# Performance work log

Measured on AMD Instinct MI355X. Metric: run time of the kernel, lower is better.

## Reference

```python
import jax, jax.numpy as jnp
import numpy as np

B, N, H, A, S = 8, 8192, 256, 64, 32  # batch, nodes, hidden, annotation, sub_graphs


def _mysoftmax(x):
    # exp, zero out where x <= 0, normalize over last dim, nan (0/0) -> 0
    x_exp = jnp.where(x > 0, jnp.exp(x), 0.0)
    part = jnp.sum(x_exp, axis=-1, keepdims=True)
    # safe divide: where partition == 0 the faithful result after nan_to_num is 0
    return jnp.where(part > 0, x_exp / jnp.where(part > 0, part, 1.0), 0.0)


def setup_inputs() -> dict:
    key = jax.random.key(0)
    k1, k2, k3, k4, k5, k6 = jax.random.split(key, 6)
    x = jax.random.normal(k1, (B, N, H + A), dtype=jnp.float32)
    node_map = jax.random.uniform(k2, (B, S, N), dtype=jnp.float32)
    lim = 1.0 / np.sqrt(H + A)
    Wi = jax.random.uniform(k3, (H, H + A), minval=-lim, maxval=lim, dtype=jnp.float32)
    bi = jax.random.uniform(k4, (H,), minval=-lim, maxval=lim, dtype=jnp.float32)
    Wj = jax.random.uniform(k5, (H, H + A), minval=-lim, maxval=lim, dtype=jnp.float32)
    bj = jax.random.uniform(k6, (H,), minval=-lim, maxval=lim, dtype=jnp.float32)
    return {"x": x, "node_map": node_map, "Wi": Wi, "bi": bi, "Wj": Wj, "bj": bj}


def reference(x, node_map, Wi, bi, Wj, bj):
    # gated node features: sigmoid(fc_i(x)) * tanh(fc_j(x))  -> [B, N, H]
    x_sigm = jax.nn.sigmoid(jnp.einsum('bnf,hf->bnh', x, Wi) + bi)
    x_tanh = jnp.tanh(jnp.einsum('bnf,hf->bnh', x, Wj) + bj)
    x_all = x_sigm * x_tanh
    # per-node L2 norm -> [B, 1, N]
    x_norm = jnp.linalg.norm(x_all, axis=-1)[:, None, :]
    # scaled subgraph map and masked softmax over nodes -> [B, S, N]
    weight = _mysoftmax(node_map * x_norm)
    # weighted sum over nodes (replaces [B,S,N,H] broadcast) -> [B, S, H]
    pooled = jnp.einsum('bsn,bnh->bsh', weight, x_all)
    return jnp.tanh(pooled), weight[..., None]
```

## Files before the change

### kernel.cpp

```cpp
#include <hip/hip_runtime.h>
#include <cstdint>
#include <cstddef>

typedef unsigned short u16;
typedef unsigned int   u32;
using short8 = __attribute__((ext_vector_type(8))) short;
using f32x4  = __attribute__((ext_vector_type(4))) float;

#define NB    8
#define NN    8192
#define HH    256
#define FF    320
#define SS    32
#define NROWS 65536
#define NCH   32

__device__ __forceinline__ u16 f2bf(float f) {
    union { float f; u32 u; } v; v.f = f;
    u32 r = v.u + 0x7fffu + ((v.u >> 16) & 1u);
    return (u16)(r >> 16);
}
__device__ __forceinline__ u32 pk2(float lo, float hi) {
    u32 r;
    asm("v_cvt_pk_bf16_f32 %0, %1, %2" : "=v"(r) : "v"(lo), "v"(hi));
    return r;
}

__global__ __launch_bounds__(256) void prep_all(
    const float* __restrict__ x, const float* __restrict__ Wi,
    const float* __restrict__ Wj,
    u16* __restrict__ xb16, u16* __restrict__ Wb, float* __restrict__ normsq)
{
    int gid = blockIdx.x * 256 + threadIdx.x;
    #pragma unroll
    for (int i = 0; i < 5; ++i) {
        size_t o = (size_t)gid + (size_t)i * 524288;
        const float4* s = reinterpret_cast<const float4*>(x + o * 8);
        float4 a = s[0], b = s[1];
        union { u32 u[4]; uint4 v; } r;
        r.u[0] = pk2(a.x, a.y); r.u[1] = pk2(a.z, a.w);
        r.u[2] = pk2(b.x, b.y); r.u[3] = pk2(b.z, b.w);
        *reinterpret_cast<uint4*>(xb16 + o * 8) = r.v;
    }
    if (gid < 163840) {
        float v = (gid < 81920) ? Wi[gid] : Wj[gid - 81920];
        Wb[gid] = f2bf(v);
    }
    if (gid < NROWS) normsq[gid] = 0.f;
}

__global__ __launch_bounds__(256, 2) void gemm_gate(
    const u16* __restrict__ xb16, const u16* __restrict__ Wb,
    const float* __restrict__ bi, const float* __restrict__ bj,
    u16* __restrict__ xa, float* __restrict__ normsq)
{
    __shared__ u16 lB[5 * 8192];

    const int bx   = blockIdx.x;
    const int xcd  = bx & 7;
    const int ht   = (bx >> 3) & 3;
    const int slot = bx >> 5;
    const int mb   = xcd + slot * 8;
    const int m0   = mb * 256;
    const int h0   = ht * 64;
    const int b_idx = m0 >> 13;
    const int n0    = m0 & 8191;

    const int tid  = threadIdx.x;
    const int w    = tid >> 6;
    const int lane = tid & 63;
    const int quad = lane >> 4;
    const int l15  = lane & 15;

    {
        const int rsub = lane >> 3;
        const int kg   = (lane & 7) ^ rsub;
        #pragma unroll
        for (int kt = 0; kt < 5; ++kt) {
            #pragma unroll
            for (int j = 0; j < 4; ++j) {
                int sl  = w * 4 + j;
                int row = sl * 8 + rsub;
                int mat = row >> 6, hl = row & 63;
                const u16* gsrc = Wb + mat * 81920 + (size_t)(h0 + hl) * FF + kt * 64 + kg * 8;
                u16* ldst = &lB[kt * 8192 + sl * 512];
                __builtin_amdgcn_global_load_lds(
                    (const __attribute__((address_space(1))) void*)gsrc,
                    (__attribute__((address_space(3))) void*)ldst, 16, 0, 0);
            }
        }
    }

    const u16* xb = xb16 + (size_t)(m0 + w * 64 + l15) * FF + quad * 8;

    f32x4 acc[8][4];
    #pragma unroll
    for (int a = 0; a < 8; ++a)
        #pragma unroll
        for (int m = 0; m < 4; ++m) acc[a][m] = (f32x4){0.f, 0.f, 0.f, 0.f};

    short8 pre[4][4];
    #pragma unroll
    for (int p = 0; p < 3; ++p)
        #pragma unroll
        for (int mt = 0; mt < 4; ++mt)
            pre[p][mt] = *reinterpret_cast<const short8*>(xb + mt * 16 * FF + p * 32);

    __syncthreads();

    #pragma unroll
    for (int ks = 0; ks < 10; ++ks) {
        const int cur = ks & 3;
        if (ks < 7) {
            const int nxt = (ks + 3) & 3;
            const int f   = (ks + 3) * 32;
            #pragma unroll
            for (int mt = 0; mt < 4; ++mt)
                pre[nxt][mt] = *reinterpret_cast<const short8*>(xb + mt * 16 * FF + f);
        }
        const int kt = ks >> 1, kk = ks & 1;
        #pragma unroll
        for (int mn = 0; mn < 8; ++mn) {
            int c = mn * 16 + l15;
            short8 bv = *reinterpret_cast<const short8*>(
                &lB[kt * 8192 + c * 64 + (((kk * 4 + quad) ^ (c & 7)) << 3)]);
            #pragma unroll
            for (int mt = 0; mt < 4; ++mt)
                acc[mn][mt] = __builtin_amdgcn_mfma_f32_16x16x32_bf16(pre[cur][mt], bv, acc[mn][mt], 0, 0, 0);
        }
    }

    float s0[4][4];
    #pragma unroll
    for (int mt = 0; mt < 4; ++mt)
        #pragma unroll
        for (int r = 0; r < 4; ++r) s0[mt][r] = 0.f;

    #pragma unroll
    for (int hq = 0; hq < 4; ++hq) {
        int h = h0 + hq * 16 + l15;
        float bi_v = bi[h], bj_v = bj[h];
        #pragma unroll
        for (int mt = 0; mt < 4; ++mt) {
            float xall[4];
            #pragma unroll
            for (int r = 0; r < 4; ++r) {
                float yi = acc[hq][mt][r] + bi_v;
                float yj = acc[hq + 4][mt][r] + bj_v;
                float sg = 1.f / (1.f + __expf(-yi));
                float e2 = __expf(-2.f * yj);
                float th = (1.f - e2) / (1.f + e2);
                float xv = sg * th;
                xall[r] = xv;
                s0[mt][r] += xv * xv;
            }
            uint2 pk;
            pk.x = pk2(xall[0], xall[1]);
            pk.y = pk2(xall[2], xall[3]);
            size_t o = (size_t)b_idx * ((size_t)HH * NN) + (size_t)h * NN
                     + (size_t)(n0 + w * 64 + mt * 16 + quad * 4);
            *reinterpret_cast<uint2*>(&xa[o]) = pk;
        }
    }
    #pragma unroll
    for (int m = 1; m <= 8; m <<= 1) {
        #pragma unroll
        for (int mt = 0; mt < 4; ++mt)
            #pragma unroll
            for (int r = 0; r < 4; ++r)
                s0[mt][r] += __shfl_xor(s0[mt][r], m, 64);
    }
    if (l15 == 0) {
        #pragma unroll
        for (int mt = 0; mt < 4; ++mt)
            #pragma unroll
            for (int r = 0; r < 4; ++r)
                atomicAdd(&normsq[m0 + w * 64 + mt * 16 + quad * 4 + r], s0[mt][r]);
    }
}

__global__ __launch_bounds__(1024) void softmax_k(
    const float* __restrict__ nm, const float* __restrict__ normsq,
    float* __restrict__ out1)
{
    __shared__ float red[16];
    int bs = blockIdx.x;
    int b  = bs >> 5;
    const float* src = nm + (size_t)bs * NN;
    float* dst       = out1 + (size_t)bs * NN;
    const float* ns  = normsq + (size_t)b * NN;
    int tid = threadIdx.x;
    float e[8];
    float sum = 0.f;
    #pragma unroll
    for (int i = 0; i < 8; ++i) {
        int n = i * 1024 + tid;
        float logit = src[n] * sqrtf(ns[n]);
        float v = (logit > 0.f) ? __expf(logit) : 0.f;
        e[i] = v;
        sum += v;
    }
    #pragma unroll
    for (int m = 1; m <= 32; m <<= 1) sum += __shfl_xor(sum, m, 64);
    int w = tid >> 6, lane = tid & 63;
    if (lane == 0) red[w] = sum;
    __syncthreads();
    float part = 0.f;
    #pragma unroll
    for (int j = 0; j < 16; ++j) part += red[j];
    float inv = (part > 0.f) ? (1.f / part) : 0.f;
    #pragma unroll
    for (int i = 0; i < 8; ++i) dst[i * 1024 + tid] = e[i] * inv;
}

__global__ __launch_bounds__(256) void pooled_k(
    const u16* __restrict__ xa, const float* __restrict__ wgt,
    float* __restrict__ part)
{
    __shared__ u16 lw[32 * 264];
    int bx = blockIdx.x;
    int ht = bx >> 8;
    int bc = bx & 255;
    int b  = bc >> 5, c = bc & 31;
    int n0 = c * 256;
    int tid = threadIdx.x, w = tid >> 6, lane = tid & 63, quad = lane >> 4, l15 = lane & 15;

    {
        int s  = tid >> 3;
        int nb = (tid & 7) * 32;
        const float* src = wgt + (size_t)(b * SS + s) * NN + n0 + nb;
        #pragma unroll
        for (int q = 0; q < 8; ++q) {
            float4 v = *reinterpret_cast<const float4*>(src + q * 4);
            uint2 pk;
            pk.x = pk2(v.x, v.y);
            pk.y = pk2(v.z, v.w);
            *reinterpret_cast<uint2*>(&lw[s * 264 + nb + q * 4]) = pk;
        }
    }
    __syncthreads();

    f32x4 acc[2];
    acc[0] = (f32x4){0.f, 0.f, 0.f, 0.f};
    acc[1] = (f32x4){0.f, 0.f, 0.f, 0.f};

    const u16* ab = xa + (size_t)b * ((size_t)HH * NN)
                  + (size_t)(ht * 64 + w * 16 + l15) * NN + n0;
    #pragma unroll
    for (int ks = 0; ks < 8; ++ks) {
        short8 av = *reinterpret_cast<const short8*>(ab + ks * 32 + quad * 8);
        #pragma unroll
        for (int st = 0; st < 2; ++st) {
            int s = st * 16 + l15;
            short8 bv = *reinterpret_cast<const short8*>(&lw[s * 264 + ks * 32 + quad * 8]);
            acc[st] = __builtin_amdgcn_mfma_f32_16x16x32_bf16(av, bv, acc[st], 0, 0, 0);
        }
    }
    float* pb = part + (size_t)(b * NCH + c) * 8192;
    #pragma unroll
    for (int st = 0; st < 2; ++st) {
        int h = ht * 64 + w * 16 + quad * 4;
        int s = st * 16 + l15;
        *reinterpret_cast<f32x4*>(&pb[s * 256 + h]) = acc[st];
    }
}

__global__ __launch_bounds__(256) void reduce_tanh(const float* __restrict__ part,
                                                   float* __restrict__ out0)
{
    int gid = blockIdx.x * 256 + threadIdx.x;
    int b = gid >> 13, r = gid & 8191;
    const float* p = part + (size_t)b * NCH * 8192 + r;
    float s = 0.f;
    #pragma unroll
    for (int c = 0; c < NCH; ++c) s += p[(size_t)c * 8192];
    out0[gid] = tanhf(s);
}

extern "C" void kernel_launch(void* const* d_in, const int* in_sizes, int n_in,
                              void* d_out, int out_size, void* d_ws, size_t ws_size,
                              hipStream_t stream) {
    const float* x  = (const float*)d_in[0];
    const float* nm = (const float*)d_in[1];
    const float* Wi = (const float*)d_in[2];
    const float* bi = (const float*)d_in[3];
    const float* Wj = (const float*)d_in[4];
    const float* bj = (const float*)d_in[5];
    float* out0 = (float*)d_out;
    float* out1 = out0 + NB * SS * HH;

    char* ws = (char*)d_ws;
    u16*   Wb     = (u16*)ws;
    u16*   xb16   = (u16*)(ws + 327680);
    u16*   xa     = (u16*)(ws + 327680 + 41943040);
    float* normsq = (float*)(ws + 327680 + 41943040 + 33554432);
    float* part   = (float*)(ws + 327680 + 41943040 + 33554432 + 262144);

    prep_all   <<<2048, 256, 0, stream>>>(x, Wi, Wj, xb16, Wb, normsq);
    gemm_gate  <<<1024, 256, 0, stream>>>(xb16, Wb, bi, bj, xa, normsq);
    softmax_k  <<<256, 1024, 0, stream>>>(nm, normsq, out1);
    pooled_k   <<<1024, 256, 0, stream>>>(xa, out1, part);
    reduce_tanh<<<256,  256, 0, stream>>>(part, out0);
}
```

Before: 199.5 us.

## Emit bf16 softmax weights once and read them directly in pooled kernel

The softmax kernel now also writes a bf16 copy of the weights, and switches to contiguous 8-element float4 loads and stores per thread. The pooled kernel reads those bf16 weights straight from global memory as MFMA operands, with no LDS staging, no per-block fp32-to-bf16 conversion and no __syncthreads. Before, the weights were read four times as fp32 (once per h-tile block). The cost is an extra workspace buffer, an extra write in softmax, and uncached-pattern global loads for the B operand in pooled_k.

New measurement: 204.8 us. +2.7%, slower.

```diff
diff --git a/kernel.cpp b/kernel.cpp
--- a/kernel.cpp
+++ b/kernel.cpp
@@ -181,21 +181,28 @@
 
 __global__ __launch_bounds__(1024) void softmax_k(
     const float* __restrict__ nm, const float* __restrict__ normsq,
-    float* __restrict__ out1)
+    float* __restrict__ out1, u16* __restrict__ wgtb)
 {
     __shared__ float red[16];
     int bs = blockIdx.x;
     int b  = bs >> 5;
     const float* src = nm + (size_t)bs * NN;
     float* dst       = out1 + (size_t)bs * NN;
+    u16* dstb        = wgtb + (size_t)bs * NN;
     const float* ns  = normsq + (size_t)b * NN;
     int tid = threadIdx.x;
+    int n0  = tid * 8;
     float e[8];
     float sum = 0.f;
+    float4 s0v = *reinterpret_cast<const float4*>(src + n0);
+    float4 s1v = *reinterpret_cast<const float4*>(src + n0 + 4);
+    float4 q0v = *reinterpret_cast<const float4*>(ns + n0);
+    float4 q1v = *reinterpret_cast<const float4*>(ns + n0 + 4);
+    float sv[8] = {s0v.x, s0v.y, s0v.z, s0v.w, s1v.x, s1v.y, s1v.z, s1v.w};
+    float qv[8] = {q0v.x, q0v.y, q0v.z, q0v.w, q1v.x, q1v.y, q1v.z, q1v.w};
     #pragma unroll
     for (int i = 0; i < 8; ++i) {
-        int n = i * 1024 + tid;
-        float logit = src[n] * sqrtf(ns[n]);
+        float logit = sv[i] * sqrtf(qv[i]);
         float v = (logit > 0.f) ? __expf(logit) : 0.f;
         e[i] = v;
         sum += v;
@@ -209,15 +216,21 @@
     #pragma unroll
     for (int j = 0; j < 16; ++j) part += red[j];
     float inv = (part > 0.f) ? (1.f / part) : 0.f;
-    #pragma unroll
-    for (int i = 0; i < 8; ++i) dst[i * 1024 + tid] = e[i] * inv;
+    float o[8];
+    #pragma unroll
+    for (int i = 0; i < 8; ++i) o[i] = e[i] * inv;
+    *reinterpret_cast<float4*>(dst + n0)     = (float4){o[0], o[1], o[2], o[3]};
+    *reinterpret_cast<float4*>(dst + n0 + 4) = (float4){o[4], o[5], o[6], o[7]};
+    union { u32 u[4]; uint4 v; } pk;
+    pk.u[0] = pk2(o[0], o[1]); pk.u[1] = pk2(o[2], o[3]);
+    pk.u[2] = pk2(o[4], o[5]); pk.u[3] = pk2(o[6], o[7]);
+    *reinterpret_cast<uint4*>(dstb + n0) = pk.v;
 }
 
 __global__ __launch_bounds__(256) void pooled_k(
-    const u16* __restrict__ xa, const float* __restrict__ wgt,
+    const u16* __restrict__ xa, const u16* __restrict__ wgtb,
     float* __restrict__ part)
 {
-    __shared__ u16 lw[32 * 264];
     int bx = blockIdx.x;
     int ht = bx >> 8;
     int bc = bx & 255;
@@ -225,36 +238,22 @@
     int n0 = c * 256;
     int tid = threadIdx.x, w = tid >> 6, lane = tid & 63, quad = lane >> 4, l15 = lane & 15;
 
-    {
-        int s  = tid >> 3;
-        int nb = (tid & 7) * 32;
-        const float* src = wgt + (size_t)(b * SS + s) * NN + n0 + nb;
-        #pragma unroll
-        for (int q = 0; q < 8; ++q) {
-            float4 v = *reinterpret_cast<const float4*>(src + q * 4);
-            uint2 pk;
-            pk.x = pk2(v.x, v.y);
-            pk.y = pk2(v.z, v.w);
-            *reinterpret_cast<uint2*>(&lw[s * 264 + nb + q * 4]) = pk;
-        }
-    }
-    __syncthreads();
-
     f32x4 acc[2];
     acc[0] = (f32x4){0.f, 0.f, 0.f, 0.f};
     acc[1] = (f32x4){0.f, 0.f, 0.f, 0.f};
 
     const u16* ab = xa + (size_t)b * ((size_t)HH * NN)
                   + (size_t)(ht * 64 + w * 16 + l15) * NN + n0;
+    const u16* wb0 = wgtb + (size_t)(b * SS + l15) * NN + n0;
+    const u16* wb1 = wgtb + (size_t)(b * SS + 16 + l15) * NN + n0;
     #pragma unroll
     for (int ks = 0; ks < 8; ++ks) {
-        short8 av = *reinterpret_cast<const short8*>(ab + ks * 32 + quad * 8);
-        #pragma unroll
-        for (int st = 0; st < 2; ++st) {
-            int s = st * 16 + l15;
-            short8 bv = *reinterpret_cast<const short8*>(&lw[s * 264 + ks * 32 + quad * 8]);
-            acc[st] = __builtin_amdgcn_mfma_f32_16x16x32_bf16(av, bv, acc[st], 0, 0, 0);
-        }
+        int ko = ks * 32 + quad * 8;
+        short8 av  = *reinterpret_cast<const short8*>(ab  + ko);
+        short8 bv0 = *reinterpret_cast<const short8*>(wb0 + ko);
+        short8 bv1 = *reinterpret_cast<const short8*>(wb1 + ko);
+        acc[0] = __builtin_amdgcn_mfma_f32_16x16x32_bf16(av, bv0, acc[0], 0, 0, 0);
+        acc[1] = __builtin_amdgcn_mfma_f32_16x16x32_bf16(av, bv1, acc[1], 0, 0, 0);
     }
     float* pb = part + (size_t)(b * NCH + c) * 8192;
     #pragma unroll
@@ -295,10 +294,11 @@
     u16*   xa     = (u16*)(ws + 327680 + 41943040);
     float* normsq = (float*)(ws + 327680 + 41943040 + 33554432);
     float* part   = (float*)(ws + 327680 + 41943040 + 33554432 + 262144);
+    u16*   wgtb   = (u16*)(ws + 327680 + 41943040 + 33554432 + 262144 + 8388608);
 
     prep_all   <<<2048, 256, 0, stream>>>(x, Wi, Wj, xb16, Wb, normsq);
     gemm_gate  <<<1024, 256, 0, stream>>>(xb16, Wb, bi, bj, xa, normsq);
-    softmax_k  <<<256, 1024, 0, stream>>>(nm, normsq, out1);
-    pooled_k   <<<1024, 256, 0, stream>>>(xa, out1, part);
+    softmax_k  <<<256, 1024, 0, stream>>>(nm, normsq, out1, wgtb);
+    pooled_k   <<<1024, 256, 0, stream>>>(xa, wgtb, part);
     reduce_tanh<<<256,  256, 0, stream>>>(part, out0);
 }
```
